# Optimization experiments

Measured on AMD Instinct MI355X. Metric: run time of the kernel, lower is better.

The kernel has to match this reference:

```python
import jax, jax.numpy as jnp
import numpy as np

HIDDEN = 4096
IN_DIM = 784
OUT_DIM = 10
CF = 4  # compression_factor
BATCH = 8192


def _dequant_weight(tile_i32, alphas, out_dim, in_dim):
    """Reconstruct weight: tile (+1/-1, size numel/CF) repeated CF times,
    each repetition (tile_size chunk) scaled by its own alpha, reshaped to [out,in].
    Since chunk i of the tiled vector is exactly the tile, this is alphas[i]*sign."""
    sign = (2 * tile_i32 - 1).astype(alphas.dtype)            # [tile_size], +/-1
    flat = (alphas[:, None] * sign[None, :]).reshape(-1)      # [numel]
    return flat.reshape(out_dim, in_dim)


def setup_inputs() -> dict:
    key = jax.random.key(0)
    k1, k2, k3, k4, k5 = jax.random.split(key, 5)
    x = jax.random.normal(k1, (BATCH, IN_DIM), dtype=jnp.float32)
    tile1 = jax.random.randint(k2, (HIDDEN * IN_DIM // CF,), 0, 2, dtype=jnp.int32)
    alphas1 = jax.random.uniform(k3, (CF,), dtype=jnp.float32)
    tile2 = jax.random.randint(k4, (OUT_DIM * HIDDEN // CF,), 0, 2, dtype=jnp.int32)
    alphas2 = jax.random.uniform(k5, (CF,), dtype=jnp.float32)
    return {"x": x, "tile1": tile1, "alphas1": alphas1, "tile2": tile2, "alphas2": alphas2}


def reference(x, tile1, alphas1, tile2, alphas2):
    w1 = _dequant_weight(tile1, alphas1, HIDDEN, IN_DIM)   # [4096, 784]
    h = jax.nn.relu(x @ w1.T)                              # [B, 4096]
    # NOTE: original forward redundantly recomputes fc1's dequantized weight
    # here and discards it; that is dead code (no effect on output), omitted.
    w2 = _dequant_weight(tile2, alphas2, OUT_DIM, HIDDEN)  # [10, 4096]
    out = h @ w2.T                                         # [B, 10]
    return out
```

## Files before the change

kernel.cpp:

```cpp
#include <hip/hip_runtime.h>

#define B_    8192
#define K_    784
#define KP    896
#define NKT   7
#define RP    1024
#define HID   4096
#define OD    10
#define TS2   10240

#define NB_XQ 1792
#define NB_SQ 224
#define NB_F  64
#define NB_Z  80

typedef __attribute__((ext_vector_type(8))) short  bf16x8;
typedef __attribute__((ext_vector_type(4))) int    i32x4;
typedef __attribute__((ext_vector_type(4))) float  f32x4;

__device__ __forceinline__ unsigned short f2bf(float f) {
    unsigned u = __builtin_bit_cast(unsigned, f);
    u += 0x7fffu + ((u >> 16) & 1u);
    return (unsigned short)(u >> 16);
}
__device__ __forceinline__ int qz32(float v) {
    v = fminf(fmaxf(v * 32.f, -127.f), 127.f);
    return (int)__builtin_rintf(v);
}

__global__ __launch_bounds__(256) void prep(
    const float* __restrict__ x, const int* __restrict__ t1,
    const int* __restrict__ t2, const float* __restrict__ a1,
    const float* __restrict__ a2,
    signed char* __restrict__ Xq, signed char* __restrict__ Sq,
    unsigned short* __restrict__ Vfrag, float* __restrict__ out)
{
    const int b = blockIdx.x;
    if (b < NB_XQ) {
        const int id  = b * 256 + threadIdx.x;
        const int row = id / 56;
        const int rem = id - row * 56;
        const int kb  = rem >> 2;
        const int s   = rem & 3;
        const int xi  = (row >> 1) & 3;
        const int k0  = kb * 64 + ((s ^ xi) << 4);
        i32x4 w = {0, 0, 0, 0};
        if (k0 < K_) {
            const float* xp = x + (size_t)row * K_ + k0;
            #pragma unroll
            for (int g = 0; g < 4; ++g) {
                f32x4 a = *(const f32x4*)(xp + g * 4);
                const int q0 = qz32(a.x), q1 = qz32(a.y);
                const int q2 = qz32(a.z), q3 = qz32(a.w);
                w[g] = (q0 & 255) | ((q1 & 255) << 8) |
                       ((q2 & 255) << 16) | ((q3 & 255) << 24);
            }
        }
        *(i32x4*)(Xq + (size_t)row * KP + kb * 64 + s * 16) = w;
    } else if (b < NB_XQ + NB_SQ) {
        const int id  = (b - NB_XQ) * 256 + threadIdx.x;
        const int row = id / 56;
        const int rem = id - row * 56;
        const int kb  = rem >> 2;
        const int s   = rem & 3;
        const int xi  = (row >> 1) & 3;
        const int k0  = kb * 64 + ((s ^ xi) << 4);
        i32x4 w = {0, 0, 0, 0};
        if (k0 < K_) {
            const int* tp = t1 + (size_t)row * K_ + k0;
            #pragma unroll
            for (int g = 0; g < 4; ++g) {
                int wg = 0;
                #pragma unroll
                for (int j = 0; j < 4; ++j)
                    wg |= (tp[g * 4 + j] ? 0x01 : 0xFF) << (8 * j);
                w[g] = wg;
            }
        }
        *(i32x4*)(Sq + (size_t)row * KP + kb * 64 + s * 16) = w;
    } else if (b < NB_XQ + NB_SQ + NB_F) {
        const int id = (b - NB_XQ - NB_SQ) * 256 + threadIdx.x;
        const int o = id >> 10;
        const int r = id & 1023;
        float v = 0.f;
        if (o < OD) {
            #pragma unroll
            for (int c = 0; c < 4; ++c) {
                const int idx = o * HID + c * RP + r;
                const int ch  = idx / TS2;
                const float w2v = a2[ch] * (float)(2 * t2[idx - ch * TS2] - 1);
                v = fmaf(a1[c], w2v, v);
            }
        }
        Vfrag[(r >> 5) * 512 + (o + 16 * ((r >> 3) & 3)) * 8 + (r & 7)] = f2bf(v);
    } else {
        const int id = (b - NB_XQ - NB_SQ - NB_F) * 256 + threadIdx.x;
        ((f32x4*)out)[id] = (f32x4){0.f, 0.f, 0.f, 0.f};
    }
}

__global__ __launch_bounds__(256, 2) void gemm1(const signed char* __restrict__ Xq,
                                                const signed char* __restrict__ Sq,
                                                const unsigned short* __restrict__ Vfrag,
                                                float* __restrict__ out) {
    __shared__ unsigned char SH[65536];

    const int tid  = threadIdx.x;
    const int lane = tid & 63;
    const int wid  = tid >> 6;

    const int swz = (blockIdx.x & 7) * 64 + (blockIdx.x >> 3);
    const int bm  = (swz >> 3) * 128;
    const int bn  = (swz & 7) * 128;

    const int wr = (wid >> 1) * 64;
    const int wc = (wid & 1) * 64;

    const int srow = lane >> 2;
    const int sslt = (lane & 3) << 4;

    const int kg   = lane >> 4;
    const int xr   = ((lane & 15) >> 1) & 3;
    const int fsl  = (kg ^ xr) << 4;
    const int frow = lane & 15;

    i32x4 acc[4][4] = {};

#define STAGE(T, BUF)                                                           \
    do {                                                                        \
        _Pragma("unroll")                                                       \
        for (int i = 0; i < 2; ++i) {                                           \
            const int base = wid * 2048 + i * 1024;                             \
            const int row  = wid * 32 + i * 16 + srow;                          \
            const signed char* ga = Xq + (size_t)(bm + row) * KP + (T) * 128 + sslt; \
            const signed char* gb = Sq + (size_t)(bn + row) * KP + (T) * 128 + sslt; \
            __builtin_amdgcn_global_load_lds(                                   \
                (const __attribute__((address_space(1))) void*)ga,              \
                (__attribute__((address_space(3))) void*)                       \
                    (&SH[(BUF) * 32768 + base + lane * 16]), 16, 0, 0);         \
            __builtin_amdgcn_global_load_lds(                                   \
                (const __attribute__((address_space(1))) void*)(ga + 64),       \
                (__attribute__((address_space(3))) void*)                       \
                    (&SH[(BUF) * 32768 + 8192 + base + lane * 16]), 16, 0, 0);  \
            __builtin_amdgcn_global_load_lds(                                   \
                (const __attribute__((address_space(1))) void*)gb,              \
                (__attribute__((address_space(3))) void*)                       \
                    (&SH[(BUF) * 32768 + 16384 + base + lane * 16]), 16, 0, 0); \
            __builtin_amdgcn_global_load_lds(                                   \
                (const __attribute__((address_space(1))) void*)(gb + 64),       \
                (__attribute__((address_space(3))) void*)                       \
                    (&SH[(BUF) * 32768 + 24576 + base + lane * 16]), 16, 0, 0); \
        }                                                                       \
    } while (0)

#define COMPUTE(BUF)                                                            \
    do {                                                                        \
        _Pragma("unroll")                                                       \
        for (int half = 0; half < 2; ++half) {                                  \
            i32x4 af[4], bfr[4];                                                \
            _Pragma("unroll")                                                   \
            for (int mi = 0; mi < 4; ++mi)                                      \
                af[mi] = *(const i32x4*)&SH[(BUF) * 32768 + half * 8192         \
                                            + (wr + mi * 16 + frow) * 64 + fsl];\
            _Pragma("unroll")                                                   \
            for (int ni = 0; ni < 4; ++ni)                                      \
                bfr[ni] = *(const i32x4*)&SH[(BUF) * 32768 + 16384 + half * 8192\
                                             + (wc + ni * 16 + frow) * 64 + fsl];\
            _Pragma("unroll")                                                   \
            for (int mi = 0; mi < 4; ++mi)                                      \
                _Pragma("unroll")                                               \
                for (int ni = 0; ni < 4; ++ni)                                  \
                    acc[mi][ni] = __builtin_amdgcn_mfma_i32_16x16x64_i8(        \
                        af[mi], bfr[ni], acc[mi][ni], 0, 0, 0);                 \
        }                                                                       \
    } while (0)

    STAGE(0, 0);

    for (int t = 0; t < NKT; ++t) {
        const int cur = t & 1;
        if (t + 1 < NKT) {
            STAGE(t + 1, cur ^ 1);
            asm volatile("s_waitcnt vmcnt(8)" ::: "memory");
        } else {
            asm volatile("s_waitcnt vmcnt(0)" ::: "memory");
        }
        __builtin_amdgcn_s_barrier();
        __builtin_amdgcn_sched_barrier(0);
        COMPUTE(cur);
        __builtin_amdgcn_sched_barrier(0);
        __builtin_amdgcn_s_barrier();
    }
#undef STAGE
#undef COMPUTE

    unsigned short* Hlds = (unsigned short*)SH;
    __syncthreads();
    #pragma unroll
    for (int mi = 0; mi < 4; ++mi) {
        #pragma unroll
        for (int ni = 0; ni < 4; ++ni) {
            const int col = wc + ni * 16 + (lane & 15);
            #pragma unroll
            for (int r = 0; r < 4; ++r) {
                const int row = wr + mi * 16 + (lane >> 4) * 4 + r;
                const float hv = (float)acc[mi][ni][r] * 0.03125f;
                Hlds[row * 128 + ((((col >> 3) ^ (row & 7)) << 3) | (col & 7))]
                    = f2bf(fmaxf(hv, 0.f));
            }
        }
    }
    __syncthreads();

    const int kb0 = bn >> 5;
    bf16x8 vb[4];
    #pragma unroll
    for (int kk = 0; kk < 4; ++kk)
        vb[kk] = *(const bf16x8*)&Vfrag[(kb0 + kk) * 512 + lane * 8];

    #pragma unroll
    for (int mf = 0; mf < 2; ++mf) {
        const int mloc = (wid * 2 + mf) * 16;
        const int mrow = mloc + (lane & 15);
        f32x4 pac = {};
        #pragma unroll
        for (int kk = 0; kk < 4; ++kk) {
            const int slot = kk * 4 + (lane >> 4);
            bf16x8 ha = *(const bf16x8*)&Hlds[mrow * 128 + ((slot ^ (mrow & 7)) << 3)];
            pac = __builtin_amdgcn_mfma_f32_16x16x32_bf16(ha, vb[kk], pac, 0, 0, 0);
        }
        const int o = lane & 15;
        if (o < OD) {
            #pragma unroll
            for (int r = 0; r < 4; ++r) {
                const int rowg = bm + mloc + (lane >> 4) * 4 + r;
                atomicAdd(&out[(size_t)rowg * OD + o], pac[r]);
            }
        }
    }
}

#define BM 128
#define BN 128
#define BK 16
__global__ __launch_bounds__(256, 2) void fused_tilednn(
    const float* __restrict__ x, const int* __restrict__ tile1,
    const float* __restrict__ alphas1, const int* __restrict__ tile2,
    const float* __restrict__ alphas2, float* __restrict__ out)
{
    __shared__ float XsF[BK][BM];
    __shared__ float SsF[BK][BN];
    __shared__ float Vl[OD][BN];
    const int t = threadIdx.x, tx = t & 15, ty = t >> 4;
    const int bm = blockIdx.x * BM, bn = blockIdx.y * BN;
    for (int e = t; e < OD * BN; e += 256) {
        const int o = e / BN, rl = e - o * BN, rr = bn + rl;
        float v = 0.f;
        #pragma unroll
        for (int c = 0; c < 4; ++c) {
            const int idx = o * HID + c * RP + rr;
            const int ch = idx / TS2;
            v = fmaf(alphas1[c], alphas2[ch] * (float)(2 * tile2[idx - ch * TS2] - 1), v);
        }
        Vl[o][rl] = v;
    }
    float acc[8][8];
    #pragma unroll
    for (int i = 0; i < 8; ++i)
        #pragma unroll
        for (int j = 0; j < 8; ++j) acc[i][j] = 0.f;
    const int lr = t >> 1, lk = (t & 1) << 3;
    const float* xrow = x + (size_t)(bm + lr) * K_;
    const int* srow = tile1 + (size_t)(bn + lr) * K_;
    for (int k0 = 0; k0 < K_; k0 += BK) {
        __syncthreads();
        const float4 xa = *(const float4*)(xrow + k0 + lk);
        const float4 xb = *(const float4*)(xrow + k0 + lk + 4);
        const int4 sa = *(const int4*)(srow + k0 + lk);
        const int4 sb = *(const int4*)(srow + k0 + lk + 4);
        XsF[lk+0][lr]=xa.x; XsF[lk+1][lr]=xa.y; XsF[lk+2][lr]=xa.z; XsF[lk+3][lr]=xa.w;
        XsF[lk+4][lr]=xb.x; XsF[lk+5][lr]=xb.y; XsF[lk+6][lr]=xb.z; XsF[lk+7][lr]=xb.w;
        SsF[lk+0][lr]=(float)(2*sa.x-1); SsF[lk+1][lr]=(float)(2*sa.y-1);
        SsF[lk+2][lr]=(float)(2*sa.z-1); SsF[lk+3][lr]=(float)(2*sa.w-1);
        SsF[lk+4][lr]=(float)(2*sb.x-1); SsF[lk+5][lr]=(float)(2*sb.y-1);
        SsF[lk+6][lr]=(float)(2*sb.z-1); SsF[lk+7][lr]=(float)(2*sb.w-1);
        __syncthreads();
        #pragma unroll
        for (int k = 0; k < BK; ++k) {
            float av[8], bv[8];
            #pragma unroll
            for (int i = 0; i < 8; ++i) av[i] = XsF[k][ty*8+i];
            #pragma unroll
            for (int j = 0; j < 8; ++j) bv[j] = SsF[k][tx*8+j];
            #pragma unroll
            for (int i = 0; i < 8; ++i)
                #pragma unroll
                for (int j = 0; j < 8; ++j) acc[i][j] = fmaf(av[i], bv[j], acc[i][j]);
        }
    }
    #pragma unroll
    for (int i = 0; i < 8; ++i)
        #pragma unroll
        for (int j = 0; j < 8; ++j) acc[i][j] = fmaxf(acc[i][j], 0.f);
    #pragma unroll
    for (int o = 0; o < OD; ++o) {
        float vv[8];
        #pragma unroll
        for (int j = 0; j < 8; ++j) vv[j] = Vl[o][tx*8+j];
        float p[8];
        #pragma unroll
        for (int i = 0; i < 8; ++i) {
            float s = 0.f;
            #pragma unroll
            for (int j = 0; j < 8; ++j) s = fmaf(acc[i][j], vv[j], s);
            p[i] = s;
        }
        #pragma unroll
        for (int m = 8; m >= 1; m >>= 1)
            #pragma unroll
            for (int i = 0; i < 8; ++i) p[i] += __shfl_xor(p[i], m, 16);
        if (tx == 0) {
            #pragma unroll
            for (int i = 0; i < 8; ++i)
                atomicAdd(&out[(size_t)(bm + ty*8 + i) * OD + o], p[i]);
        }
    }
}

extern "C" void kernel_launch(void* const* d_in, const int* in_sizes, int n_in,
                              void* d_out, int out_size, void* d_ws, size_t ws_size,
                              hipStream_t stream) {
    const float* x       = (const float*)d_in[0];
    const int*   tile1   = (const int*)  d_in[1];
    const float* alphas1 = (const float*)d_in[2];
    const int*   tile2   = (const int*)  d_in[3];
    const float* alphas2 = (const float*)d_in[4];
    float*       out     = (float*)d_out;

    const size_t OFF_XQ = 0;
    const size_t OFF_SQ = OFF_XQ + (size_t)B_ * KP;
    const size_t OFF_F  = OFF_SQ + (size_t)RP * KP;
    const size_t NEED   = OFF_F + (size_t)16 * RP * 2;

    if (ws_size < NEED) {
        hipMemsetAsync(out, 0, (size_t)out_size * sizeof(float), stream);
        dim3 grid(B_ / BM, RP / BN);
        fused_tilednn<<<grid, 256, 0, stream>>>(x, tile1, alphas1, tile2, alphas2, out);
        return;
    }

    signed char*    Xq    = (signed char*)((char*)d_ws + OFF_XQ);
    signed char*    Sq    = (signed char*)((char*)d_ws + OFF_SQ);
    unsigned short* Vfrag = (unsigned short*)((char*)d_ws + OFF_F);

    prep<<<NB_XQ + NB_SQ + NB_F + NB_Z, 256, 0, stream>>>(
        x, tile1, tile2, alphas1, alphas2, Xq, Sq, Vfrag, out);
    gemm1<<<512, 256, 0, stream>>>(Xq, Sq, Vfrag, out);
}
```

Baseline: 25.45 us.

## Fuse activation int8 quantization into GEMM A-tile loading

Drops the separate prep pass that quantized x to int8 in global workspace. The GEMM now loads fp32 x tiles into registers one k-step ahead, quantizes them in-kernel and writes the swizzled int8 tiles to LDS, while the sign-weight tile still streams through global_load_lds double buffering. This removes a full write and re-read of the quantized activations. In exchange it adds register pressure and VALU work inside the main loop. Each of the eight column blocks sharing a row block now reads fp32 x, four times the bytes of the int8 copy.

```diff
diff --git a/kernel.cpp b/kernel.cpp
--- a/kernel.cpp
+++ b/kernel.cpp
@@ -2,14 +2,13 @@
 
 #define B_    8192
 #define K_    784
-#define KP    896
+#define KPS   896
 #define NKT   7
 #define RP    1024
 #define HID   4096
 #define OD    10
 #define TS2   10240
 
-#define NB_XQ 1792
 #define NB_SQ 224
 #define NB_F  64
 #define NB_Z  80
@@ -29,14 +28,13 @@
 }
 
 __global__ __launch_bounds__(256) void prep(
-    const float* __restrict__ x, const int* __restrict__ t1,
-    const int* __restrict__ t2, const float* __restrict__ a1,
-    const float* __restrict__ a2,
-    signed char* __restrict__ Xq, signed char* __restrict__ Sq,
-    unsigned short* __restrict__ Vfrag, float* __restrict__ out)
+    const int* __restrict__ t1, const int* __restrict__ t2,
+    const float* __restrict__ a1, const float* __restrict__ a2,
+    signed char* __restrict__ Sq, unsigned short* __restrict__ Vfrag,
+    float* __restrict__ out)
 {
     const int b = blockIdx.x;
-    if (b < NB_XQ) {
+    if (b < NB_SQ) {
         const int id  = b * 256 + threadIdx.x;
         const int row = id / 56;
         const int rem = id - row * 56;
@@ -46,27 +44,6 @@
         const int k0  = kb * 64 + ((s ^ xi) << 4);
         i32x4 w = {0, 0, 0, 0};
         if (k0 < K_) {
-            const float* xp = x + (size_t)row * K_ + k0;
-            #pragma unroll
-            for (int g = 0; g < 4; ++g) {
-                f32x4 a = *(const f32x4*)(xp + g * 4);
-                const int q0 = qz32(a.x), q1 = qz32(a.y);
-                const int q2 = qz32(a.z), q3 = qz32(a.w);
-                w[g] = (q0 & 255) | ((q1 & 255) << 8) |
-                       ((q2 & 255) << 16) | ((q3 & 255) << 24);
-            }
-        }
-        *(i32x4*)(Xq + (size_t)row * KP + kb * 64 + s * 16) = w;
-    } else if (b < NB_XQ + NB_SQ) {
-        const int id  = (b - NB_XQ) * 256 + threadIdx.x;
-        const int row = id / 56;
-        const int rem = id - row * 56;
-        const int kb  = rem >> 2;
-        const int s   = rem & 3;
-        const int xi  = (row >> 1) & 3;
-        const int k0  = kb * 64 + ((s ^ xi) << 4);
-        i32x4 w = {0, 0, 0, 0};
-        if (k0 < K_) {
             const int* tp = t1 + (size_t)row * K_ + k0;
             #pragma unroll
             for (int g = 0; g < 4; ++g) {
@@ -77,9 +54,9 @@
                 w[g] = wg;
             }
         }
-        *(i32x4*)(Sq + (size_t)row * KP + kb * 64 + s * 16) = w;
-    } else if (b < NB_XQ + NB_SQ + NB_F) {
-        const int id = (b - NB_XQ - NB_SQ) * 256 + threadIdx.x;
+        *(i32x4*)(Sq + (size_t)row * KPS + kb * 64 + s * 16) = w;
+    } else if (b < NB_SQ + NB_F) {
+        const int id = (b - NB_SQ) * 256 + threadIdx.x;
         const int o = id >> 10;
         const int r = id & 1023;
         float v = 0.f;
@@ -94,12 +71,12 @@
         }
         Vfrag[(r >> 5) * 512 + (o + 16 * ((r >> 3) & 3)) * 8 + (r & 7)] = f2bf(v);
     } else {
-        const int id = (b - NB_XQ - NB_SQ - NB_F) * 256 + threadIdx.x;
+        const int id = (b - NB_SQ - NB_F) * 256 + threadIdx.x;
         ((f32x4*)out)[id] = (f32x4){0.f, 0.f, 0.f, 0.f};
     }
 }
 
-__global__ __launch_bounds__(256, 2) void gemm1(const signed char* __restrict__ Xq,
+__global__ __launch_bounds__(256, 2) void gemm1(const float* __restrict__ x,
                                                 const signed char* __restrict__ Sq,
                                                 const unsigned short* __restrict__ Vfrag,
                                                 float* __restrict__ out) {
@@ -116,40 +93,69 @@
     const int wr = (wid >> 1) * 64;
     const int wc = (wid & 1) * 64;
 
-    const int srow = lane >> 2;
-    const int sslt = (lane & 3) << 4;
-
     const int kg   = lane >> 4;
     const int xr   = ((lane & 15) >> 1) & 3;
     const int fsl  = (kg ^ xr) << 4;
     const int frow = lane & 15;
 
+    const int hq  = wid >> 1;
+    const int rq  = (wid & 1) * 64 + (lane >> 2);
+    const int sq  = lane & 3;
+
     i32x4 acc[4][4] = {};
-
-#define STAGE(T, BUF)                                                           \
+    f32x4 regF[16];
+
+#define STAGE_B(T, BUF)                                                         \
     do {                                                                        \
         _Pragma("unroll")                                                       \
         for (int i = 0; i < 2; ++i) {                                           \
-            const int base = wid * 2048 + i * 1024;                             \
-            const int row  = wid * 32 + i * 16 + srow;                          \
-            const signed char* ga = Xq + (size_t)(bm + row) * KP + (T) * 128 + sslt; \
-            const signed char* gb = Sq + (size_t)(bn + row) * KP + (T) * 128 + sslt; \
-            __builtin_amdgcn_global_load_lds(                                   \
-                (const __attribute__((address_space(1))) void*)ga,              \
-                (__attribute__((address_space(3))) void*)                       \
-                    (&SH[(BUF) * 32768 + base + lane * 16]), 16, 0, 0);         \
-            __builtin_amdgcn_global_load_lds(                                   \
-                (const __attribute__((address_space(1))) void*)(ga + 64),       \
-                (__attribute__((address_space(3))) void*)                       \
-                    (&SH[(BUF) * 32768 + 8192 + base + lane * 16]), 16, 0, 0);  \
+            const int row = wid * 32 + i * 16 + (lane >> 2);                    \
+            const signed char* gb = Sq + (size_t)(bn + row) * KPS               \
+                                       + (T) * 128 + (lane & 3) * 16;           \
             __builtin_amdgcn_global_load_lds(                                   \
                 (const __attribute__((address_space(1))) void*)gb,              \
                 (__attribute__((address_space(3))) void*)                       \
-                    (&SH[(BUF) * 32768 + 16384 + base + lane * 16]), 16, 0, 0); \
+                    (&SH[32768 + (BUF) * 16384 + wid * 2048 + i * 1024 + lane * 16]), \
+                16, 0, 0);                                                      \
             __builtin_amdgcn_global_load_lds(                                   \
                 (const __attribute__((address_space(1))) void*)(gb + 64),       \
                 (__attribute__((address_space(3))) void*)                       \
-                    (&SH[(BUF) * 32768 + 24576 + base + lane * 16]), 16, 0, 0); \
+                    (&SH[32768 + (BUF) * 16384 + 8192 + wid * 2048 + i * 1024 + lane * 16]), \
+                16, 0, 0);                                                      \
+        }                                                                       \
+    } while (0)
+
+#define LOAD_AF32(T)                                                            \
+    do {                                                                        \
+        _Pragma("unroll")                                                       \
+        for (int j = 0; j < 4; ++j) {                                           \
+            const int row = rq + j * 16;                                        \
+            const int c   = (T) * 128 + hq * 64 + ((sq ^ ((row >> 1) & 3)) << 4); \
+            const float* p = x + (size_t)(bm + row) * K_ + (c < K_ ? c : 0);    \
+            _Pragma("unroll")                                                   \
+            for (int g = 0; g < 4; ++g)                                         \
+                regF[j * 4 + g] = *(const f32x4*)(p + g * 4);                   \
+        }                                                                       \
+    } while (0)
+
+#define QUANT_WRITE(T, BUF)                                                     \
+    do {                                                                        \
+        _Pragma("unroll")                                                       \
+        for (int j = 0; j < 4; ++j) {                                           \
+            const int row = rq + j * 16;                                        \
+            const int c   = (T) * 128 + hq * 64 + ((sq ^ ((row >> 1) & 3)) << 4); \
+            i32x4 w = {0, 0, 0, 0};                                             \
+            if (c < K_) {                                                       \
+                _Pragma("unroll")                                               \
+                for (int g = 0; g < 4; ++g) {                                   \
+                    f32x4 a = regF[j * 4 + g];                                  \
+                    const int q0 = qz32(a.x), q1 = qz32(a.y);                   \
+                    const int q2 = qz32(a.z), q3 = qz32(a.w);                   \
+                    w[g] = (q0 & 255) | ((q1 & 255) << 8) |                     \
+                           ((q2 & 255) << 16) | ((q3 & 255) << 24);             \
+                }                                                               \
+            }                                                                   \
+            *(i32x4*)(&SH[(BUF) * 16384 + wid * 4096 + j * 1024 + lane * 16]) = w; \
         }                                                                       \
     } while (0)
 
@@ -160,11 +166,11 @@
             i32x4 af[4], bfr[4];                                                \
             _Pragma("unroll")                                                   \
             for (int mi = 0; mi < 4; ++mi)                                      \
-                af[mi] = *(const i32x4*)&SH[(BUF) * 32768 + half * 8192         \
+                af[mi] = *(const i32x4*)&SH[(BUF) * 16384 + half * 8192         \
                                             + (wr + mi * 16 + frow) * 64 + fsl];\
             _Pragma("unroll")                                                   \
             for (int ni = 0; ni < 4; ++ni)                                      \
-                bfr[ni] = *(const i32x4*)&SH[(BUF) * 32768 + 16384 + half * 8192\
+                bfr[ni] = *(const i32x4*)&SH[32768 + (BUF) * 16384 + half * 8192\
                                              + (wc + ni * 16 + frow) * 64 + fsl];\
             _Pragma("unroll")                                                   \
             for (int mi = 0; mi < 4; ++mi)                                      \
@@ -175,23 +181,31 @@
         }                                                                       \
     } while (0)
 
-    STAGE(0, 0);
-
+    STAGE_B(0, 0);
+    LOAD_AF32(0);
+
+    #pragma unroll
     for (int t = 0; t < NKT; ++t) {
         const int cur = t & 1;
         if (t + 1 < NKT) {
-            STAGE(t + 1, cur ^ 1);
-            asm volatile("s_waitcnt vmcnt(8)" ::: "memory");
+            STAGE_B(t + 1, cur ^ 1);
+            asm volatile("s_waitcnt vmcnt(4)" ::: "memory");
         } else {
             asm volatile("s_waitcnt vmcnt(0)" ::: "memory");
         }
+        QUANT_WRITE(t, cur);
+        asm volatile("s_waitcnt lgkmcnt(0)" ::: "memory");
+        __builtin_amdgcn_sched_barrier(0);
         __builtin_amdgcn_s_barrier();
         __builtin_amdgcn_sched_barrier(0);
         COMPUTE(cur);
+        if (t + 1 < NKT) LOAD_AF32(t + 1);
         __builtin_amdgcn_sched_barrier(0);
         __builtin_amdgcn_s_barrier();
     }
-#undef STAGE
+#undef STAGE_B
+#undef LOAD_AF32
+#undef QUANT_WRITE
 #undef COMPUTE
 
     unsigned short* Hlds = (unsigned short*)SH;
@@ -337,9 +351,8 @@
     const float* alphas2 = (const float*)d_in[4];
     float*       out     = (float*)d_out;
 
-    const size_t OFF_XQ = 0;
-    const size_t OFF_SQ = OFF_XQ + (size_t)B_ * KP;
-    const size_t OFF_F  = OFF_SQ + (size_t)RP * KP;
+    const size_t OFF_SQ = 0;
+    const size_t OFF_F  = OFF_SQ + (size_t)RP * KPS;
     const size_t NEED   = OFF_F + (size_t)16 * RP * 2;
 
     if (ws_size < NEED) {
@@ -349,11 +362,10 @@
         return;
     }
 
-    signed char*    Xq    = (signed char*)((char*)d_ws + OFF_XQ);
     signed char*    Sq    = (signed char*)((char*)d_ws + OFF_SQ);
     unsigned short* Vfrag = (unsigned short*)((char*)d_ws + OFF_F);
 
-    prep<<<NB_XQ + NB_SQ + NB_F + NB_Z, 256, 0, stream>>>(
-        x, tile1, tile2, alphas1, alphas2, Xq, Sq, Vfrag, out);
-    gemm1<<<512, 256, 0, stream>>>(Xq, Sq, Vfrag, out);
-}
+    prep<<<NB_SQ + NB_F + NB_Z, 256, 0, stream>>>(
+        tile1, tile2, alphas1, alphas2, Sq, Vfrag, out);
+    gemm1<<<512, 256, 0, stream>>>(x, Sq, Vfrag, out);
+}
```

After: 36.76 us. +44.5%, slower.
